# Optimization experiments

Hardware: AMD Instinct MI355X
Metric: run time of the kernel (lower is better)

## Reference

```python
import jax, jax.numpy as jnp
import numpy as np

B, T, C, H = 4, 2048, 1024, 16
D = C // H
EPS = 1e-5


def setup_inputs() -> dict:
    key = jax.random.key(0)
    ks = jax.random.split(key, 8)
    s = 0.02
    return {
        "hidden_states": jax.random.normal(ks[0], (B, T, C), jnp.float32),
        "w_attn": jax.random.normal(ks[1], (C, 3 * C), jnp.float32) * s,
        "b_attn": jnp.zeros((3 * C,), jnp.float32),
        "w_proj": jax.random.normal(ks[2], (C, C), jnp.float32) * s,
        "b_proj": jnp.zeros((C,), jnp.float32),
        "ln1_g": jnp.ones((C,), jnp.float32),
        "ln1_b": jnp.zeros((C,), jnp.float32),
        "ln2_g": jnp.ones((C,), jnp.float32),
        "ln2_b": jnp.zeros((C,), jnp.float32),
        "w_fc": jax.random.normal(ks[3], (C, 4 * C), jnp.float32) * s,
        "b_fc": jnp.zeros((4 * C,), jnp.float32),
        "w_fc2": jax.random.normal(ks[4], (4 * C, C), jnp.float32) * s,
        "b_fc2": jnp.zeros((C,), jnp.float32),
    }


def _layernorm(x, g, b):
    mu = jnp.mean(x, axis=-1, keepdims=True)
    var = jnp.mean(jnp.square(x - mu), axis=-1, keepdims=True)
    return (x - mu) * jax.lax.rsqrt(var + EPS) * g + b


def _attention(x, w_attn, b_attn, w_proj, b_proj):
    Bx, Tx, Cx = x.shape
    qkv = x @ w_attn + b_attn  # [B,T,3C]  (GCLinear transpose=True => x @ W)
    q, k, v = jnp.split(qkv, 3, axis=-1)
    # [B,T,C] -> [B,H,T,D]
    q = q.reshape(Bx, Tx, H, D).transpose(0, 2, 1, 3)
    k = k.reshape(Bx, Tx, H, D).transpose(0, 2, 1, 3)
    v = v.reshape(Bx, Tx, H, D).transpose(0, 2, 1, 3)
    att = jnp.einsum("bhqd,bhkd->bhqk", q, k) * (1.0 / np.sqrt(D))
    causal = jnp.tril(jnp.ones((Tx, Tx), bool))
    att = jnp.where(causal, att, -jnp.inf)
    att = jax.nn.softmax(att, axis=-1)
    y = jnp.einsum("bhqk,bhkd->bhqd", att, v)
    y = y.transpose(0, 2, 1, 3).reshape(Bx, Tx, Cx)
    return y @ w_proj + b_proj


def reference(hidden_states, w_attn, b_attn, w_proj, b_proj,
              ln1_g, ln1_b, ln2_g, ln2_b, w_fc, b_fc, w_fc2, b_fc2):
    x = hidden_states
    a = _attention(_layernorm(x, ln1_g, ln1_b), w_attn, b_attn, w_proj, b_proj)
    x = x + a
    h = _layernorm(x, ln2_g, ln2_b)
    h = jax.nn.gelu(h @ w_fc + b_fc, approximate=False)  # nn.GELU default = exact erf
    h = h @ w_fc2 + b_fc2
    return x + h
```

## Files before the change

kernel.cpp:

```cpp
#include <hip/hip_runtime.h>
#include <hip/hip_bf16.h>
#include <stdint.h>

typedef __bf16 bf16_t;
typedef __bf16 bf16x8 __attribute__((ext_vector_type(8)));
typedef __bf16 bf16x4 __attribute__((ext_vector_type(4)));
typedef float f32x4 __attribute__((ext_vector_type(4)));
typedef short short4v __attribute__((ext_vector_type(4)));

#define BDIM_B 4
#define TDIM 2048
#define CDIM 1024

__device__ __forceinline__ void gload16(const void* g, void* l) {
  using GP = const __attribute__((address_space(1))) char*;
  using LP = __attribute__((address_space(3))) char*;
  __builtin_amdgcn_global_load_lds((GP)(uintptr_t)g, (LP)(uint32_t)(uintptr_t)l, 16, 0, 0);
}

#define S_BARRIER() asm volatile("s_barrier" ::: "memory")

__global__ __launch_bounds__(256)
void transpose_cast(const float* __restrict__ W, bf16_t* __restrict__ Wt, int K, int N) {
  __shared__ float tile[32][33];
  const int tx = threadIdx.x & 31, ty = threadIdx.x >> 5;
  const int n0 = blockIdx.x * 32, k0 = blockIdx.y * 32;
#pragma unroll
  for (int j = 0; j < 32; j += 8)
    tile[ty + j][tx] = W[(size_t)(k0 + ty + j) * N + n0 + tx];
  __syncthreads();
#pragma unroll
  for (int j = 0; j < 32; j += 8)
    Wt[(size_t)(n0 + ty + j) * K + k0 + tx] = (bf16_t)tile[tx][ty + j];
}

__global__ __launch_bounds__(256)
void ln_kernel(const float* __restrict__ x, const float* __restrict__ g,
               const float* __restrict__ bta, bf16_t* __restrict__ out) {
  const size_t row = blockIdx.x;
  const int tid = threadIdx.x;
  const float4 v = ((const float4*)(x + row * CDIM))[tid];
  float s = v.x + v.y + v.z + v.w;
#pragma unroll
  for (int off = 1; off < 64; off <<= 1) s += __shfl_xor(s, off);
  __shared__ float r1[4], r2[4];
  const int wv = tid >> 6, lane = tid & 63;
  if (!lane) r1[wv] = s;
  __syncthreads();
  const float mu = (r1[0] + r1[1] + r1[2] + r1[3]) * (1.f / CDIM);
  const float dx = v.x - mu, dy = v.y - mu, dz = v.z - mu, dw = v.w - mu;
  float q = dx * dx + dy * dy + dz * dz + dw * dw;
#pragma unroll
  for (int off = 1; off < 64; off <<= 1) q += __shfl_xor(q, off);
  if (!lane) r2[wv] = q;
  __syncthreads();
  const float var = (r2[0] + r2[1] + r2[2] + r2[3]) * (1.f / CDIM);
  const float rs = rsqrtf(var + 1e-5f);
  const float4 gg = ((const float4*)g)[tid];
  const float4 bb = ((const float4*)bta)[tid];
  bf16x4 o;
  o[0] = (bf16_t)(dx * rs * gg.x + bb.x);
  o[1] = (bf16_t)(dy * rs * gg.y + bb.y);
  o[2] = (bf16_t)(dz * rs * gg.z + bb.z);
  o[3] = (bf16_t)(dw * rs * gg.w + bb.w);
  ((bf16x4*)(out + row * CDIM))[tid] = o;
}

enum { EPI_BF16 = 0, EPI_RESID = 1, EPI_GELU = 2 };

template <int EPI>
__global__ __launch_bounds__(512)
void gemm256(const bf16_t* __restrict__ A, const bf16_t* __restrict__ Bt,
             const float* __restrict__ bias, const float* __restrict__ resid,
             void* __restrict__ outv, int M, int N, int K) {
  __shared__ bf16_t sA[2][256 * 64];
  __shared__ bf16_t sB[2][256 * 64];
  const int tid = threadIdx.x;
  const int lane = tid & 63, wv = tid >> 6;
  const int wm = wv >> 2, wn = wv & 3;
  const int rin = lane & 15, quad = lane >> 4;

  const int nwg = gridDim.x * gridDim.y;
  const int bid = blockIdx.y * gridDim.x + blockIdx.x;
  const int swzb = (bid & 7) * (nwg >> 3) + (bid >> 3);
  const int bx = swzb % gridDim.x, by = swzb / gridDim.x;
  const int m0 = by * 256, n0 = bx * 256;

  const int c8 = (lane & 7) ^ ((lane >> 3) & 7);
  const int aRow = wm * 128 + (wv & 3) * 8 + (lane >> 3);
  const int bRow = wn * 64 + (wv >> 2) * 8 + (lane >> 3);
  const bf16_t* srcA = A + (size_t)(m0 + aRow) * K + c8 * 8;
  const bf16_t* srcB = Bt + (size_t)(n0 + bRow) * K + c8 * 8;
  const int dstA = (wm * 128 + (wv & 3) * 8) * 64;
  const int dstB = (wn * 64 + (wv >> 2) * 8) * 64;

#define STA(buf, r, kk) gload16(srcA + (size_t)(32 * (r)) * K + (kk), (buf) + dstA + 32 * (r) * 64)
#define STB(buf, r, kk) gload16(srcB + (size_t)(16 * (r)) * K + (kk), (buf) + dstB + 16 * (r) * 64)

  const int ck0 = (quad ^ (rin & 7)) * 8;
  const int ck1 = ((4 + quad) ^ (rin & 7)) * 8;
  const int aBase = (wm * 128 + rin) * 64;
  const int bBase = (wn * 64 + rin) * 64;

  f32x4 acc[8][4] = {};
  bf16x8 af[8][2], bfr[4][2];

#define RDA(mi) { af[mi][0] = *(const bf16x8*)(rA + aBase + (mi)*1024 + ck0); \
                  af[mi][1] = *(const bf16x8*)(rA + aBase + (mi)*1024 + ck1); }
#define RDB(ni) { bfr[ni][0] = *(const bf16x8*)(rB + bBase + (ni)*1024 + ck0); \
                  bfr[ni][1] = *(const bf16x8*)(rB + bBase + (ni)*1024 + ck1); }
#define MM(mi, ni) { acc[mi][ni] = __builtin_amdgcn_mfma_f32_16x16x32_bf16(af[mi][0], bfr[ni][0], acc[mi][ni], 0, 0, 0); \
                     acc[mi][ni] = __builtin_amdgcn_mfma_f32_16x16x32_bf16(af[mi][1], bfr[ni][1], acc[mi][ni], 0, 0, 0); }

  const int NT = K >> 6;

  STA(sA[0], 0, 0); STB(sB[0], 0, 0); STB(sB[0], 1, 0);
  STA(sA[0], 1, 0); STB(sB[0], 2, 0); STB(sB[0], 3, 0);
  STA(sA[0], 2, 0);
  STA(sA[0], 3, 0);
  asm volatile("s_waitcnt vmcnt(5)" ::: "memory");
  S_BARRIER();

  for (int t = 0; t < NT; ++t) {
    const bf16_t* rA = sA[t & 1];
    const bf16_t* rB = sB[t & 1];
    bf16_t* wA = sA[(t & 1) ^ 1];
    bf16_t* wB = sB[(t & 1) ^ 1];
    const int kk = (t + 1 < NT ? t + 1 : t) * 64;

    RDA(0) RDA(1) RDB(0) RDB(1)
    asm volatile("s_waitcnt vmcnt(2)" ::: "memory");
    S_BARRIER();
    STA(wA, 0, kk); STB(wB, 0, kk); STB(wB, 1, kk);
    __builtin_amdgcn_s_setprio(1);
    MM(0, 0) MM(0, 1) MM(1, 0) MM(1, 1)
    __builtin_amdgcn_s_setprio(0);

    RDA(2) RDA(3) RDB(2) RDB(3)
    asm volatile("s_waitcnt vmcnt(4)" ::: "memory");
    S_BARRIER();
    STA(wA, 1, kk); STB(wB, 2, kk); STB(wB, 3, kk);
    __builtin_amdgcn_s_setprio(1);
    MM(0, 2) MM(0, 3) MM(1, 2) MM(1, 3) MM(2, 0) MM(2, 1) MM(3, 0) MM(3, 1)
    __builtin_amdgcn_s_setprio(0);

    RDA(4) RDA(5)
    asm volatile("s_waitcnt vmcnt(6)" ::: "memory");
    S_BARRIER();
    STA(wA, 2, kk);
    __builtin_amdgcn_s_setprio(1);
    MM(2, 2) MM(2, 3) MM(3, 2) MM(3, 3) MM(4, 0) MM(4, 1) MM(5, 0) MM(5, 1)
    __builtin_amdgcn_s_setprio(0);

    RDA(6) RDA(7)
    asm volatile("s_waitcnt vmcnt(4)" ::: "memory");
    S_BARRIER();
    STA(wA, 3, kk);
    __builtin_amdgcn_s_setprio(1);
    MM(4, 2) MM(4, 3) MM(5, 2) MM(5, 3) MM(6, 0) MM(6, 1) MM(7, 0) MM(7, 1)
    MM(6, 2) MM(6, 3) MM(7, 2) MM(7, 3)
    __builtin_amdgcn_s_setprio(0);
  }
  asm volatile("s_waitcnt vmcnt(0)" ::: "memory");

  const int rbase = m0 + wm * 128 + quad * 4;
  const int cbase = n0 + wn * 64 + rin;
#pragma unroll
  for (int mi = 0; mi < 8; ++mi)
#pragma unroll
    for (int ni = 0; ni < 4; ++ni)
#pragma unroll
      for (int r = 0; r < 4; ++r) {
        const int m = rbase + mi * 16 + r;
        const int n = cbase + ni * 16;
        float v = acc[mi][ni][r] + bias[n];
        if (EPI == EPI_RESID) v += resid[(size_t)m * N + n];
        if (EPI == EPI_GELU) v = 0.5f * v * (1.0f + erff(v * 0.7071067811865476f));
        if (EPI == EPI_RESID)
          ((float*)outv)[(size_t)m * N + n] = v;
        else
          ((bf16_t*)outv)[(size_t)m * N + n] = (bf16_t)v;
      }
#undef STA
#undef STB
#undef RDA
#undef RDB
#undef MM
}

template <int EPI>
__global__ __launch_bounds__(512)
void gemm128(const bf16_t* __restrict__ A, const bf16_t* __restrict__ Bt,
             const float* __restrict__ bias, const float* __restrict__ resid,
             void* __restrict__ outv, int M, int N, int K) {
  __shared__ bf16_t sA[3][256 * 64];
  __shared__ bf16_t sB[3][128 * 64];
  const int tid = threadIdx.x;
  const int lane = tid & 63, wv = tid >> 6;
  const int wm = wv >> 1, wn = wv & 1;
  const int rin = lane & 15, quad = lane >> 4;

  const int nwg = gridDim.x * gridDim.y;
  const int bid = blockIdx.y * gridDim.x + blockIdx.x;
  const int swzb = (bid & 7) * (nwg >> 3) + (bid >> 3);
  const int bx = swzb % gridDim.x, by = swzb / gridDim.x;
  const int m0 = by * 256, n0 = bx * 128;

  const int c8 = (lane & 7) ^ ((lane >> 3) & 7);
  const bf16_t* srcA = A + (size_t)(m0 + 8 * wv + (lane >> 3)) * K + c8 * 8;
  const int dstA = (8 * wv) * 64;
  const bf16_t* srcB = Bt + (size_t)(n0 + (wv >> 2) * 64 + (wv & 3) * 8 + (lane >> 3)) * K + c8 * 8;
  const int dstB = ((wv >> 2) * 64 + (wv & 3) * 8) * 64;

#define STA(buf, r, kk) gload16(srcA + (size_t)(64 * (r)) * K + (kk), (buf) + dstA + 64 * (r) * 64)
#define STB(buf, r, kk) gload16(srcB + (size_t)(32 * (r)) * K + (kk), (buf) + dstB + 32 * (r) * 64)

  const int ck0 = (quad ^ (rin & 7)) * 8;
  const int ck1 = ((4 + quad) ^ (rin & 7)) * 8;
  const int aBase = (wm * 64 + rin) * 64;
  const int bBase = (wn * 64 + rin) * 64;

  f32x4 acc[4][4] = {};
  bf16x8 af[4][2], bfr[4][2];

#define RDA(mi) { af[mi][0] = *(const bf16x8*)(rA + aBase + (mi)*1024 + ck0); \
                  af[mi][1] = *(const bf16x8*)(rA + aBase + (mi)*1024 + ck1); }
#define RDB(ni) { bfr[ni][0] = *(const bf16x8*)(rB + bBase + (ni)*1024 + ck0); \
                  bfr[ni][1] = *(const bf16x8*)(rB + bBase + (ni)*1024 + ck1); }
#define MM(mi, ni) { acc[mi][ni] = __builtin_amdgcn_mfma_f32_16x16x32_bf16(af[mi][0], bfr[ni][0], acc[mi][ni], 0, 0, 0); \
                     acc[mi][ni] = __builtin_amdgcn_mfma_f32_16x16x32_bf16(af[mi][1], bfr[ni][1], acc[mi][ni], 0, 0, 0); }

  const int NT = K >> 6;

  STA(sA[0], 0, 0); STA(sA[0], 1, 0); STA(sA[0], 2, 0); STA(sA[0], 3, 0); STB(sB[0], 0, 0);
  STB(sB[0], 1, 0);
  STA(sA[1], 0, 64); STA(sA[1], 1, 64); STA(sA[1], 2, 64); STA(sA[1], 3, 64); STB(sB[1], 0, 64);
  STB(sB[1], 1, 64);
  asm volatile("s_waitcnt vmcnt(7)" ::: "memory");
  S_BARRIER();

  int rb = 0, wb = 2;
  for (int t = 0; t < NT; ++t) {
    const bf16_t* rA = sA[rb];
    const bf16_t* rB = sB[rb];
    bf16_t* wA = sA[wb];
    bf16_t* wB = sB[wb];
    const int kk = (t + 2 < NT ? t + 2 : NT - 1) * 64;

    RDA(0) RDA(1) RDA(2) RDA(3) RDB(0) RDB(1)
    asm volatile("s_waitcnt vmcnt(6)" ::: "memory");
    S_BARRIER();
    STA(wA, 0, kk); STA(wA, 1, kk); STA(wA, 2, kk); STA(wA, 3, kk); STB(wB, 0, kk);
    __builtin_amdgcn_s_setprio(1);
    MM(0, 0) MM(0, 1) MM(1, 0) MM(1, 1) MM(2, 0) MM(2, 1) MM(3, 0) MM(3, 1)
    __builtin_amdgcn_s_setprio(0);

    RDB(2) RDB(3)
    asm volatile("s_waitcnt vmcnt(6)" ::: "memory");
    S_BARRIER();
    STB(wB, 1, kk);
    __builtin_amdgcn_s_setprio(1);
    MM(0, 2) MM(0, 3) MM(1, 2) MM(1, 3) MM(2, 2) MM(2, 3) MM(3, 2) MM(3, 3)
    __builtin_amdgcn_s_setprio(0);

    rb = (rb == 2) ? 0 : rb + 1;
    wb = (wb == 2) ? 0 : wb + 1;
  }
  asm volatile("s_waitcnt vmcnt(0)" ::: "memory");

  const int rbase = m0 + wm * 64 + quad * 4;
  const int cbase = n0 + wn * 64 + rin;
#pragma unroll
  for (int mi = 0; mi < 4; ++mi)
#pragma unroll
    for (int ni = 0; ni < 4; ++ni)
#pragma unroll
      for (int r = 0; r < 4; ++r) {
        const int m = rbase + mi * 16 + r;
        const int n = cbase + ni * 16;
        float v = acc[mi][ni][r] + bias[n];
        if (EPI == EPI_RESID) v += resid[(size_t)m * N + n];
        if (EPI == EPI_GELU) v = 0.5f * v * (1.0f + erff(v * 0.7071067811865476f));
        if (EPI == EPI_RESID)
          ((float*)outv)[(size_t)m * N + n] = v;
        else
          ((bf16_t*)outv)[(size_t)m * N + n] = (bf16_t)v;
      }
#undef STA
#undef STB
#undef RDA
#undef RDB
#undef MM
}

__global__ __launch_bounds__(256)
void attn_kernel(const bf16_t* __restrict__ qkv, bf16_t* __restrict__ y) {
  const int h = blockIdx.y, b = blockIdx.z;
  const int tid = threadIdx.x, lane = tid & 63, wv = tid >> 6;
  const int rin = lane & 15, quad = lane >> 4;

  __shared__ bf16_t Kt[64 * 64];
  __shared__ bf16_t Vt[64 * 64];

  const size_t base3 = (size_t)(b * TDIM) * 3072;
  const int srow = tid >> 2, sseg = tid & 3;
  const short4v ones = {(short)0x3F80, (short)0x3F80, (short)0x3F80, (short)0x3F80};

#pragma unroll 1
  for (int seg = 0; seg < 2; ++seg) {
    const int qt = seg ? blockIdx.x : (15 - blockIdx.x);
    const int q0 = qt * 128;
    const int nkt = qt * 2 + 2;

    bf16x8 aq[2][2];
#pragma unroll
    for (int qf = 0; qf < 2; ++qf) {
      const size_t qr = base3 + (size_t)(q0 + wv * 32 + qf * 16 + rin) * 3072 + h * 64;
#pragma unroll
      for (int ki = 0; ki < 2; ++ki)
        aq[qf][ki] = *(const bf16x8*)(qkv + qr + ki * 32 + quad * 8);
    }

    uint4 kreg[2], vreg[2];
#pragma unroll
    for (int hf = 0; hf < 2; ++hf) {
      const size_t gb = base3 + (size_t)srow * 3072 + h * 64 + hf * 32 + sseg * 8;
      kreg[hf] = *(const uint4*)(qkv + gb + 1024);
      vreg[hf] = *(const uint4*)(qkv + gb + 2048);
    }

    f32x4 o[2][4] = {};
    f32x4 ol[2] = {};

    for (int kt = 0; kt < nkt; ++kt) {
      __syncthreads();
      {
        const int krot = (srow >> 2) & 7;
        const int tg = srow >> 3, to = srow & 7;
#pragma unroll
        for (int hf = 0; hf < 2; ++hf) {
          const int g = hf * 4 + sseg;
          *(uint4*)(Kt + srow * 64 + (((g + krot) & 7) * 8)) = kreg[hf];
          union { uint4 u; bf16_t e[8]; } vv;
          vv.u = vreg[hf];
#pragma unroll
          for (int j = 0; j < 8; ++j) {
            const int d = hf * 32 + sseg * 8 + j;
            Vt[d * 64 + (((tg + ((d >> 2) & 7)) & 7) * 8) + to] = vv.e[j];
          }
        }
      }
      __syncthreads();
      {
        const int ktn = (kt + 1 < nkt) ? kt + 1 : kt;
#pragma unroll
        for (int hf = 0; hf < 2; ++hf) {
          const size_t gb = base3 + (size_t)(ktn * 64 + srow) * 3072 + h * 64 + hf * 32 + sseg * 8;
          kreg[hf] = *(const uint4*)(qkv + gb + 1024);
          vreg[hf] = *(const uint4*)(qkv + gb + 2048);
        }
      }
      f32x4 st[2][4] = {};
#pragma unroll
      for (int ki = 0; ki < 2; ++ki) {
        bf16x8 ak[4];
#pragma unroll
        for (int kf = 0; kf < 4; ++kf) {
          const int tr = kf * 16 + rin;
          ak[kf] = *(const bf16x8*)(Kt + tr * 64 + (((ki * 4 + quad + ((tr >> 2) & 7)) & 7) * 8));
        }
#pragma unroll
        for (int qf = 0; qf < 2; ++qf)
#pragma unroll
          for (int kf = 0; kf < 4; ++kf)
            st[qf][kf] = __builtin_amdgcn_mfma_f32_16x16x32_bf16(ak[kf], aq[qf][ki], st[qf][kf], 0, 0, 0);
      }
      const bool maskt = (kt >= 2 * qt);
      short4v pf[2][4];
#pragma unroll
      for (int qf = 0; qf < 2; ++qf) {
        const int qg = q0 + wv * 32 + qf * 16 + rin;
#pragma unroll
        for (int kf = 0; kf < 4; ++kf)
#pragma unroll
          for (int r = 0; r < 4; ++r) {
            const int kg = kt * 64 + kf * 16 + quad * 4 + r;
            float p = __builtin_amdgcn_exp2f(st[qf][kf][r] * 0.18033688f);
            if (maskt && kg > qg) p = 0.f;
            union { bf16_t bv; short sv; } cv;
            cv.bv = (bf16_t)p;
            pf[qf][kf][r] = cv.sv;
          }
      }
#pragma unroll
      for (int kf = 0; kf < 4; ++kf) {
        short4v bv[4];
#pragma unroll
        for (int nd = 0; nd < 4; ++nd) {
          const int d = nd * 16 + rin;
          const int sw = (2 * kf + (quad >> 1) + ((d >> 2) & 7)) & 7;
          bv[nd] = *(const short4v*)(Vt + d * 64 + sw * 8 + (quad & 1) * 4);
        }
#pragma unroll
        for (int qf = 0; qf < 2; ++qf) {
#pragma unroll
          for (int nd = 0; nd < 4; ++nd)
            o[qf][nd] = __builtin_amdgcn_mfma_f32_16x16x16bf16_1k(pf[qf][kf], bv[nd], o[qf][nd], 0, 0, 0);
          ol[qf] = __builtin_amdgcn_mfma_f32_16x16x16bf16_1k(pf[qf][kf], ones, ol[qf], 0, 0, 0);
        }
      }
    }

#pragma unroll
    for (int qf = 0; qf < 2; ++qf)
#pragma unroll
      for (int r = 0; r < 4; ++r) {
        const float inv = 1.0f / ol[qf][r];
        const size_t row = (size_t)b * TDIM + q0 + wv * 32 + qf * 16 + quad * 4 + r;
#pragma unroll
        for (int nd = 0; nd < 4; ++nd)
          y[row * CDIM + h * 64 + nd * 16 + rin] = (bf16_t)(o[qf][nd][r] * inv);
      }
  }
}

extern "C" void kernel_launch(void* const* d_in, const int* in_sizes, int n_in,
                              void* d_out, int out_size, void* d_ws, size_t ws_size,
                              hipStream_t stream) {
  const float* x      = (const float*)d_in[0];
  const float* w_attn = (const float*)d_in[1];
  const float* b_attn = (const float*)d_in[2];
  const float* w_proj = (const float*)d_in[3];
  const float* b_proj = (const float*)d_in[4];
  const float* ln1g   = (const float*)d_in[5];
  const float* ln1b   = (const float*)d_in[6];
  const float* ln2g   = (const float*)d_in[7];
  const float* ln2b   = (const float*)d_in[8];
  const float* w_fc   = (const float*)d_in[9];
  const float* b_fc   = (const float*)d_in[10];
  const float* w_fc2  = (const float*)d_in[11];
  const float* b_fc2  = (const float*)d_in[12];
  float* out = (float*)d_out;

  char* ws = (char*)d_ws;
  bf16_t* wTattn = (bf16_t*)(ws + 0);
  bf16_t* wTproj = (bf16_t*)(ws + 6291456);
  bf16_t* wTfc   = (bf16_t*)(ws + 8388608);
  bf16_t* wTfc2  = (bf16_t*)(ws + 16777216);
  bf16_t* xn     = (bf16_t*)(ws + 25165824);
  float*  x2     = (float*)(ws + 41943040);
  bf16_t* qkv    = (bf16_t*)(ws + 75497472);
  bf16_t* yb     = (bf16_t*)(ws + 75497472 + 50331648);
  bf16_t* hb     = (bf16_t*)(ws + 75497472);

  transpose_cast<<<dim3(96, 32), 256, 0, stream>>>(w_attn, wTattn, 1024, 3072);
  transpose_cast<<<dim3(32, 32), 256, 0, stream>>>(w_proj, wTproj, 1024, 1024);
  transpose_cast<<<dim3(128, 32), 256, 0, stream>>>(w_fc, wTfc, 1024, 4096);
  transpose_cast<<<dim3(32, 128), 256, 0, stream>>>(w_fc2, wTfc2, 4096, 1024);

  ln_kernel<<<8192, 256, 0, stream>>>(x, ln1g, ln1b, xn);
  gemm128<EPI_BF16><<<dim3(24, 32), 512, 0, stream>>>(xn, wTattn, b_attn, nullptr, qkv, 8192, 3072, 1024);
  attn_kernel<<<dim3(8, 16, 4), 256, 0, stream>>>(qkv, yb);
  gemm128<EPI_RESID><<<dim3(8, 32), 512, 0, stream>>>(yb, wTproj, b_proj, x, x2, 8192, 1024, 1024);
  ln_kernel<<<8192, 256, 0, stream>>>(x2, ln2g, ln2b, xn);
  gemm256<EPI_GELU><<<dim3(16, 32), 512, 0, stream>>>(xn, wTfc, b_fc, nullptr, hb, 8192, 4096, 1024);
  gemm128<EPI_RESID><<<dim3(8, 32), 512, 0, stream>>>(hb, wTfc2, b_fc2, x2, out, 8192, 1024, 4096);
}
```

Baseline: 511.8 us.

## Pre-transpose V and double-buffer K/V tiles via direct global-to-LDS loads

Adds a separate kernel that transposes V into a per-head [D,T] buffer, reusing the free xn workspace. The attention kernel now streams K and transposed V straight into double-buffered LDS with global_load_lds, with an XOR swizzle, so the scattered per-element V transpose through registers goes away. Query tiles shrink from 128 to 64 rows, one 16-row fragment per wave, and the grid becomes 1024 blocks for better balance across CUs. The cost is an extra kernel launch plus a round trip of V through memory, and each block does less work per K/V tile it loads.

```diff
diff --git a/kernel.cpp b/kernel.cpp
--- a/kernel.cpp
+++ b/kernel.cpp
@@ -32,6 +32,35 @@
 #pragma unroll
   for (int j = 0; j < 32; j += 8)
     Wt[(size_t)(n0 + ty + j) * K + k0 + tx] = (bf16_t)tile[tx][ty + j];
+}
+
+__global__ __launch_bounds__(256)
+void transpose_v(const bf16_t* __restrict__ qkv, bf16_t* __restrict__ vT) {
+  __shared__ bf16_t tile[64 * 64];
+  const int tt = blockIdx.x;
+  const int h = blockIdx.y, b = blockIdx.z;
+  const int tid = threadIdx.x;
+  const int sr = tid >> 3, sc = tid & 7;
+  const bf16_t* src = qkv + (size_t)(b * TDIM) * 3072 + 2048 + h * 64;
+#pragma unroll
+  for (int p = 0; p < 2; ++p) {
+    const int t = p * 32 + sr;
+    *(uint4*)(tile + t * 64 + ((sc ^ (t & 7)) * 8)) =
+        *(const uint4*)(src + (size_t)(tt * 64 + t) * 3072 + sc * 8);
+  }
+  __syncthreads();
+  const int d = tid >> 2, tq = tid & 3;
+  bf16_t* dst = vT + ((size_t)((b * 16 + h) * 64 + d)) * TDIM + tt * 64;
+#pragma unroll
+  for (int p = 0; p < 2; ++p) {
+    union { uint4 u; bf16_t e[8]; } o;
+#pragma unroll
+    for (int j = 0; j < 8; ++j) {
+      const int t = p * 32 + tq * 8 + j;
+      o.e[j] = tile[t * 64 + (((d >> 3) ^ (t & 7)) * 8) + (d & 7)];
+    }
+    *(uint4*)(dst + p * 32 + tq * 8) = o.u;
+  }
 }
 
 __global__ __launch_bounds__(256)
@@ -294,134 +323,103 @@
 }
 
 __global__ __launch_bounds__(256)
-void attn_kernel(const bf16_t* __restrict__ qkv, bf16_t* __restrict__ y) {
-  const int h = blockIdx.y, b = blockIdx.z;
+void attn_kernel(const bf16_t* __restrict__ qkv, const bf16_t* __restrict__ vT,
+                 bf16_t* __restrict__ y) {
+  const int id = blockIdx.x;
+  const int bx = id >> 6;
+  const int h = id & 15, b = (id >> 4) & 3;
   const int tid = threadIdx.x, lane = tid & 63, wv = tid >> 6;
   const int rin = lane & 15, quad = lane >> 4;
 
-  __shared__ bf16_t Kt[64 * 64];
-  __shared__ bf16_t Vt[64 * 64];
+  __shared__ bf16_t K2[2][64 * 64];
+  __shared__ bf16_t V2[2][64 * 64];
 
   const size_t base3 = (size_t)(b * TDIM) * 3072;
-  const int srow = tid >> 2, sseg = tid & 3;
+  const bf16_t* Kg = qkv + base3 + 1024 + h * 64;
+  const bf16_t* Vg = vT + (size_t)((b * 16 + h) * 64) * TDIM;
+  const int sr = tid >> 3, sc = tid & 7;
+  const int sx = (sc ^ (sr & 7)) * 8;
   const short4v ones = {(short)0x3F80, (short)0x3F80, (short)0x3F80, (short)0x3F80};
+
+#define STAGE(bi, kt_) { \
+    gload16(Kg + (size_t)((kt_) * 64 + sr) * 3072 + sx,      K2[bi] + sr * 64 + sc * 8);        \
+    gload16(Kg + (size_t)((kt_) * 64 + 32 + sr) * 3072 + sx, K2[bi] + (32 + sr) * 64 + sc * 8); \
+    gload16(Vg + (size_t)sr * TDIM + (kt_) * 64 + sx,        V2[bi] + sr * 64 + sc * 8);        \
+    gload16(Vg + (size_t)(32 + sr) * TDIM + (kt_) * 64 + sx, V2[bi] + (32 + sr) * 64 + sc * 8); }
 
 #pragma unroll 1
   for (int seg = 0; seg < 2; ++seg) {
-    const int qt = seg ? blockIdx.x : (15 - blockIdx.x);
-    const int q0 = qt * 128;
-    const int nkt = qt * 2 + 2;
-
-    bf16x8 aq[2][2];
-#pragma unroll
-    for (int qf = 0; qf < 2; ++qf) {
-      const size_t qr = base3 + (size_t)(q0 + wv * 32 + qf * 16 + rin) * 3072 + h * 64;
-#pragma unroll
-      for (int ki = 0; ki < 2; ++ki)
-        aq[qf][ki] = *(const bf16x8*)(qkv + qr + ki * 32 + quad * 8);
+    const int qt = seg ? bx : (31 - bx);
+    const int q0 = qt * 64;
+    const int nkt = qt + 1;
+
+    bf16x8 aq[2];
+    {
+      const size_t qr = base3 + (size_t)(q0 + wv * 16 + rin) * 3072 + h * 64;
+      aq[0] = *(const bf16x8*)(qkv + qr + quad * 8);
+      aq[1] = *(const bf16x8*)(qkv + qr + 32 + quad * 8);
     }
 
-    uint4 kreg[2], vreg[2];
-#pragma unroll
-    for (int hf = 0; hf < 2; ++hf) {
-      const size_t gb = base3 + (size_t)srow * 3072 + h * 64 + hf * 32 + sseg * 8;
-      kreg[hf] = *(const uint4*)(qkv + gb + 1024);
-      vreg[hf] = *(const uint4*)(qkv + gb + 2048);
-    }
-
-    f32x4 o[2][4] = {};
-    f32x4 ol[2] = {};
+    f32x4 o[4] = {};
+    f32x4 ol = {};
+
+    STAGE(0, 0)
+    asm volatile("s_waitcnt vmcnt(0)" ::: "memory");
+    S_BARRIER();
 
     for (int kt = 0; kt < nkt; ++kt) {
-      __syncthreads();
-      {
-        const int krot = (srow >> 2) & 7;
-        const int tg = srow >> 3, to = srow & 7;
-#pragma unroll
-        for (int hf = 0; hf < 2; ++hf) {
-          const int g = hf * 4 + sseg;
-          *(uint4*)(Kt + srow * 64 + (((g + krot) & 7) * 8)) = kreg[hf];
-          union { uint4 u; bf16_t e[8]; } vv;
-          vv.u = vreg[hf];
-#pragma unroll
-          for (int j = 0; j < 8; ++j) {
-            const int d = hf * 32 + sseg * 8 + j;
-            Vt[d * 64 + (((tg + ((d >> 2) & 7)) & 7) * 8) + to] = vv.e[j];
-          }
+      const bf16_t* Kb = K2[kt & 1];
+      const bf16_t* Vb = V2[kt & 1];
+      if (kt + 1 < nkt) STAGE((kt + 1) & 1, kt + 1)
+      f32x4 st[4] = {};
+#pragma unroll
+      for (int ki = 0; ki < 2; ++ki) {
+#pragma unroll
+        for (int kf = 0; kf < 4; ++kf) {
+          const bf16x8 ak = *(const bf16x8*)(Kb + (kf * 16 + rin) * 64 +
+                                             (((ki * 4 + quad) ^ (rin & 7)) * 8));
+          st[kf] = __builtin_amdgcn_mfma_f32_16x16x32_bf16(ak, aq[ki], st[kf], 0, 0, 0);
         }
       }
-      __syncthreads();
-      {
-        const int ktn = (kt + 1 < nkt) ? kt + 1 : kt;
-#pragma unroll
-        for (int hf = 0; hf < 2; ++hf) {
-          const size_t gb = base3 + (size_t)(ktn * 64 + srow) * 3072 + h * 64 + hf * 32 + sseg * 8;
-          kreg[hf] = *(const uint4*)(qkv + gb + 1024);
-          vreg[hf] = *(const uint4*)(qkv + gb + 2048);
+      const bool maskt = (kt == qt);
+      const int qg = q0 + wv * 16 + rin;
+      short4v pf[4];
+#pragma unroll
+      for (int kf = 0; kf < 4; ++kf)
+#pragma unroll
+        for (int r = 0; r < 4; ++r) {
+          const int kg = kt * 64 + kf * 16 + quad * 4 + r;
+          float p = __builtin_amdgcn_exp2f(st[kf][r] * 0.18033688f);
+          if (maskt && kg > qg) p = 0.f;
+          union { bf16_t bv; short sv; } cv;
+          cv.bv = (bf16_t)p;
+          pf[kf][r] = cv.sv;
         }
+#pragma unroll
+      for (int kf = 0; kf < 4; ++kf) {
+#pragma unroll
+        for (int nd = 0; nd < 4; ++nd) {
+          const short4v bv = *(const short4v*)(Vb + (nd * 16 + rin) * 64 +
+                                               (((kf * 2 + (quad >> 1)) ^ (rin & 7)) * 8) +
+                                               (quad & 1) * 4);
+          o[nd] = __builtin_amdgcn_mfma_f32_16x16x16bf16_1k(pf[kf], bv, o[nd], 0, 0, 0);
+        }
+        ol = __builtin_amdgcn_mfma_f32_16x16x16bf16_1k(pf[kf], ones, ol, 0, 0, 0);
       }
-      f32x4 st[2][4] = {};
-#pragma unroll
-      for (int ki = 0; ki < 2; ++ki) {
-        bf16x8 ak[4];
-#pragma unroll
-        for (int kf = 0; kf < 4; ++kf) {
-          const int tr = kf * 16 + rin;
-          ak[kf] = *(const bf16x8*)(Kt + tr * 64 + (((ki * 4 + quad + ((tr >> 2) & 7)) & 7) * 8));
-        }
-#pragma unroll
-        for (int qf = 0; qf < 2; ++qf)
-#pragma unroll
-          for (int kf = 0; kf < 4; ++kf)
-            st[qf][kf] = __builtin_amdgcn_mfma_f32_16x16x32_bf16(ak[kf], aq[qf][ki], st[qf][kf], 0, 0, 0);
-      }
-      const bool maskt = (kt >= 2 * qt);
-      short4v pf[2][4];
-#pragma unroll
-      for (int qf = 0; qf < 2; ++qf) {
-        const int qg = q0 + wv * 32 + qf * 16 + rin;
-#pragma unroll
-        for (int kf = 0; kf < 4; ++kf)
-#pragma unroll
-          for (int r = 0; r < 4; ++r) {
-            const int kg = kt * 64 + kf * 16 + quad * 4 + r;
-            float p = __builtin_amdgcn_exp2f(st[qf][kf][r] * 0.18033688f);
-            if (maskt && kg > qg) p = 0.f;
-            union { bf16_t bv; short sv; } cv;
-            cv.bv = (bf16_t)p;
-            pf[qf][kf][r] = cv.sv;
-          }
-      }
-#pragma unroll
-      for (int kf = 0; kf < 4; ++kf) {
-        short4v bv[4];
-#pragma unroll
-        for (int nd = 0; nd < 4; ++nd) {
-          const int d = nd * 16 + rin;
-          const int sw = (2 * kf + (quad >> 1) + ((d >> 2) & 7)) & 7;
-          bv[nd] = *(const short4v*)(Vt + d * 64 + sw * 8 + (quad & 1) * 4);
-        }
-#pragma unroll
-        for (int qf = 0; qf < 2; ++qf) {
-#pragma unroll
-          for (int nd = 0; nd < 4; ++nd)
-            o[qf][nd] = __builtin_amdgcn_mfma_f32_16x16x16bf16_1k(pf[qf][kf], bv[nd], o[qf][nd], 0, 0, 0);
-          ol[qf] = __builtin_amdgcn_mfma_f32_16x16x16bf16_1k(pf[qf][kf], ones, ol[qf], 0, 0, 0);
-        }
-      }
+      asm volatile("s_waitcnt vmcnt(0)" ::: "memory");
+      S_BARRIER();
     }
 
 #pragma unroll
-    for (int qf = 0; qf < 2; ++qf)
-#pragma unroll
-      for (int r = 0; r < 4; ++r) {
-        const float inv = 1.0f / ol[qf][r];
-        const size_t row = (size_t)b * TDIM + q0 + wv * 32 + qf * 16 + quad * 4 + r;
-#pragma unroll
-        for (int nd = 0; nd < 4; ++nd)
-          y[row * CDIM + h * 64 + nd * 16 + rin] = (bf16_t)(o[qf][nd][r] * inv);
-      }
+    for (int r = 0; r < 4; ++r) {
+      const float inv = 1.0f / ol[r];
+      const size_t row = (size_t)b * TDIM + q0 + wv * 16 + quad * 4 + r;
+#pragma unroll
+      for (int nd = 0; nd < 4; ++nd)
+        y[row * CDIM + h * 64 + nd * 16 + rin] = (bf16_t)(o[nd][r] * inv);
+    }
   }
+#undef STAGE
 }
 
 extern "C" void kernel_launch(void* const* d_in, const int* in_sizes, int n_in,
@@ -452,6 +450,7 @@
   bf16_t* qkv    = (bf16_t*)(ws + 75497472);
   bf16_t* yb     = (bf16_t*)(ws + 75497472 + 50331648);
   bf16_t* hb     = (bf16_t*)(ws + 75497472);
+  bf16_t* vT     = xn;
 
   transpose_cast<<<dim3(96, 32), 256, 0, stream>>>(w_attn, wTattn, 1024, 3072);
   transpose_cast<<<dim3(32, 32), 256, 0, stream>>>(w_proj, wTproj, 1024, 1024);
@@ -460,7 +459,8 @@
 
   ln_kernel<<<8192, 256, 0, stream>>>(x, ln1g, ln1b, xn);
   gemm128<EPI_BF16><<<dim3(24, 32), 512, 0, stream>>>(xn, wTattn, b_attn, nullptr, qkv, 8192, 3072, 1024);
-  attn_kernel<<<dim3(8, 16, 4), 256, 0, stream>>>(qkv, yb);
+  transpose_v<<<dim3(32, 16, 4), 256, 0, stream>>>(qkv, vT);
+  attn_kernel<<<dim3(1024), 256, 0, stream>>>(qkv, vT, yb);
   gemm128<EPI_RESID><<<dim3(8, 32), 512, 0, stream>>>(yb, wTproj, b_proj, x, x2, 8192, 1024, 1024);
   ln_kernel<<<8192, 256, 0, stream>>>(x2, ln2g, ln2b, xn);
   gemm256<EPI_GELU><<<dim3(16, 32), 512, 0, stream>>>(xn, wTfc, b_fc, nullptr, hb, 8192, 4096, 1024);
```

New measurement: 465.3 us. 9.1% less time.
